# Kernel tuning notes

Hardware: AMD Instinct MI355X
Metric: run time of the kernel (lower is better)

The kernel has to match this reference:

```python
import jax, jax.numpy as jnp
import numpy as np

N_NODES = 100000
N_EDGES = 1600000
IN_DIM = 128
HIDDEN = 128
OUT_DIM = 64


def setup_inputs() -> dict:
    key = jax.random.key(0)
    k_x, k_e, k_w1, k_b1, k_w2, k_b2 = jax.random.split(key, 6)
    x = jax.random.normal(k_x, (N_NODES, IN_DIM), dtype=jnp.float32)
    edge_index = jax.random.randint(k_e, (2, N_EDGES), 0, N_NODES, dtype=jnp.int64)
    # GCNConv weight/bias (glorot-ish scale) and final Linear head
    W1 = jax.random.normal(k_w1, (IN_DIM, HIDDEN), dtype=jnp.float32) / np.sqrt(IN_DIM)
    b1 = jnp.zeros((HIDDEN,), dtype=jnp.float32)
    W2 = jax.random.normal(k_w2, (HIDDEN, OUT_DIM), dtype=jnp.float32) / np.sqrt(HIDDEN)
    b2 = jnp.zeros((OUT_DIM,), dtype=jnp.float32)
    return {"x": x, "W1": W1, "b1": b1, "W2": W2, "b2": b2, "edge_index": edge_index}


def _gcn_conv(x, W, b, src, dst, norm, n_nodes):
    # PyG GCNConv: linear transform, then sym-normalized neighbor aggregation
    h = x @ W                                   # (N, H) dense transform
    msg = h[src] * norm[:, None]                # (E+N, H) gather + scale
    out = jax.ops.segment_sum(msg, dst, num_segments=n_nodes)  # scatter-add
    return out + b


def reference(x, W1, b1, W2, b2, edge_index):
    n = x.shape[0]
    # add self-loops (PyG GCNConv default)
    loop = jnp.arange(n, dtype=edge_index.dtype)
    src = jnp.concatenate([edge_index[0], loop])
    dst = jnp.concatenate([edge_index[1], loop])
    # symmetric normalization D^{-1/2} A D^{-1/2}
    deg = jnp.zeros((n,), dtype=x.dtype).at[dst].add(1.0)
    dinv = jnp.where(deg > 0, jax.lax.rsqrt(jnp.maximum(deg, 1.0)), 0.0)
    norm = dinv[src] * dinv[dst]

    h = _gcn_conv(x, W1, b1, src, dst, norm, n)
    h = jax.nn.relu(h)
    # dropout: identity in eval/inference mode
    return h @ W2 + b2
```

## Files before the change

### kernel.cpp

```cpp
#include <hip/hip_runtime.h>

#define N_NODES 100000
#define N_EDGES 1600000
#define IN_DIM  128
#define HIDDEN  128
#define OUT_DIM 64

#define NB_COARSE ((N_NODES + 255) / 256)
#define EPB 4096
#define NBLK_E ((N_EDGES + EPB - 1) / EPB)
#define GB1 ((N_NODES + 127) / 128)
#define CAP 5120
#define PCAP 6912

typedef __attribute__((ext_vector_type(8))) short bf8_t;
typedef __attribute__((ext_vector_type(4))) float f4_t;

__device__ __forceinline__ ushort f2b(float f) {
    unsigned int u = __float_as_uint(f);
    u += 0x7fffu + ((u >> 16) & 1u);
    return (ushort)(u >> 16);
}
__device__ __forceinline__ float b2f_lo(unsigned int u) { return __uint_as_float(u << 16); }
__device__ __forceinline__ float b2f_hi(unsigned int u) { return __uint_as_float(u & 0xffff0000u); }


__global__ __launch_bounds__(256, 2) void k_fuse1(const int* __restrict__ ei,
                                                  int* __restrict__ cursor,
                                                  unsigned int* __restrict__ part,
                                                  const float* __restrict__ x,
                                                  const float* __restrict__ W1,
                                                  ushort* __restrict__ h) {
    __shared__ __align__(16) ushort smem[2 * 128 * 136];
    int tid = threadIdx.x;

    if (blockIdx.x < NBLK_E) {
        int* lh    = (int*)smem;
        int* lbase = lh + NB_COARSE;
        for (int i = tid; i < NB_COARSE; i += 256) lh[i] = 0;
        __syncthreads();
        int e0 = blockIdx.x * EPB;
        int srcv[EPB / 256], dstv[EPB / 256];
        #pragma unroll
        for (int j = 0; j < EPB / 256; j++) {
            int e = e0 + j * 256 + tid;
            if (e < N_EDGES) {
                srcv[j] = ei[e];
                dstv[j] = ei[N_EDGES + e];
                atomicAdd(&lh[dstv[j] >> 8], 1);
            } else dstv[j] = -1;
        }
        __syncthreads();
        for (int i = tid; i < NB_COARSE; i += 256) {
            int c = lh[i];
            lbase[i] = (c > 0) ? (i * CAP + atomicAdd(&cursor[i], c)) : 0;
            lh[i] = 0;
        }
        __syncthreads();
        #pragma unroll
        for (int j = 0; j < EPB / 256; j++) {
            if (dstv[j] >= 0) {
                int b = dstv[j] >> 8;
                int pos = lbase[b] + atomicAdd(&lh[b], 1);
                part[pos] = ((unsigned int)(dstv[j] & 255) << 24) | (unsigned int)srcv[j];
            }
        }
        return;
    }

    typedef ushort (*tile_t)[136];
    tile_t As = (tile_t)smem;
    tile_t Bs = (tile_t)(smem + 128 * 136);
    int row0 = (blockIdx.x - NBLK_E) * 128;
    const int M = N_NODES;

    #pragma unroll
    for (int i = 0; i < 16; i++) {
        int li = tid + i * 256;
        int r = li >> 5, c4 = li & 31;
        int grow = row0 + r; if (grow > M - 1) grow = M - 1;
        float4 v = *(const float4*)(x + (size_t)grow * 128 + c4 * 4);
        ushort4 o;
        o.x = f2b(v.x); o.y = f2b(v.y); o.z = f2b(v.z); o.w = f2b(v.w);
        *(ushort4*)&As[r][c4 * 4] = o;
    }
    #pragma unroll
    for (int i = 0; i < 16; i++) {
        int li = tid + i * 256;
        int k = li >> 5, n4 = li & 31;
        float4 v = *(const float4*)(W1 + (size_t)k * 128 + n4 * 4);
        Bs[n4 * 4 + 0][k] = f2b(v.x);
        Bs[n4 * 4 + 1][k] = f2b(v.y);
        Bs[n4 * 4 + 2][k] = f2b(v.z);
        Bs[n4 * 4 + 3][k] = f2b(v.w);
    }
    __syncthreads();

    int wave = tid >> 6, lane = tid & 63;
    int lr = lane & 15, lq = lane >> 4;
    int wm0 = (wave & 1) * 64;
    int wn0 = (wave >> 1) * 64;

    f4_t acc[4][4];
    #pragma unroll
    for (int mi = 0; mi < 4; mi++)
        #pragma unroll
        for (int ni = 0; ni < 4; ni++) acc[mi][ni] = (f4_t){0.f, 0.f, 0.f, 0.f};

    #pragma unroll
    for (int kb = 0; kb < 4; kb++) {
        bf8_t af[4], bfr[4];
        #pragma unroll
        for (int mi = 0; mi < 4; mi++)
            af[mi] = *(const bf8_t*)&As[wm0 + mi * 16 + lr][kb * 32 + lq * 8];
        #pragma unroll
        for (int ni = 0; ni < 4; ni++)
            bfr[ni] = *(const bf8_t*)&Bs[wn0 + ni * 16 + lr][kb * 32 + lq * 8];
        #pragma unroll
        for (int mi = 0; mi < 4; mi++)
            #pragma unroll
            for (int ni = 0; ni < 4; ni++)
                acc[mi][ni] = __builtin_amdgcn_mfma_f32_16x16x32_bf16(
                    af[mi], bfr[ni], acc[mi][ni], 0, 0, 0);
    }

    #pragma unroll
    for (int mi = 0; mi < 4; mi++) {
        #pragma unroll
        for (int r = 0; r < 4; r++) {
            int row = row0 + wm0 + mi * 16 + lq * 4 + r;
            if (row < M) {
                #pragma unroll
                for (int ni = 0; ni < 4; ni++)
                    h[(size_t)row * 128 + wn0 + ni * 16 + lr] = f2b(acc[mi][ni][r]);
            }
        }
    }
}


__global__ __launch_bounds__(256) void k_csr(const unsigned int* __restrict__ part,
                                             const int* __restrict__ cursor,
                                             int* __restrict__ offs,
                                             int* __restrict__ pcnt,
                                             float* __restrict__ dinv,
                                             int* __restrict__ ssrc) {
    __shared__ int ldeg[256], lsc[256], lcur[256], sob[256];
    __shared__ unsigned int stage[CAP];
    int t = threadIdx.x;
    int b = blockIdx.x;
    int rbeg = b * CAP;
    int cnt = cursor[b];
    int node0 = b << 8;
    if (b == 0 && t == 0) dinv[N_NODES] = 0.f;
    ldeg[t] = 0;
    __syncthreads();
    for (int i = t; i < cnt; i += 256) {
        unsigned int u = part[rbeg + i];
        stage[i] = u;
        atomicAdd(&ldeg[u >> 24], 1);
    }
    __syncthreads();
    int v = ldeg[t];
    int pv = (v + 7) & ~7;
    lsc[t] = pv;
    __syncthreads();
    for (int off = 1; off < 256; off <<= 1) {
        int add = (t >= off) ? lsc[t - off] : 0;
        __syncthreads();
        lsc[t] += add;
        __syncthreads();
    }
    int ob = b * PCAP + (lsc[t] - pv);
    sob[t] = ob;
    lcur[t] = 0;
    if (node0 + t < N_NODES) {
        offs[node0 + t] = ob;
        pcnt[node0 + t] = pv;
        dinv[node0 + t] = rsqrtf((float)(v + 1));
    }
    __syncthreads();
    for (int i = t; i < cnt; i += 256) {
        unsigned int u = stage[i];
        int d = u >> 24;
        int pos = atomicAdd(&lcur[d], 1);
        ssrc[sob[d] + pos] = (int)(u & 0xFFFFFFu);
    }
    for (int i = v; i < pv; i++) ssrc[ob + i] = N_NODES;
}


__global__ __launch_bounds__(256) void k_agg(const ushort* __restrict__ h,
                                             const int* __restrict__ offs,
                                             const int* __restrict__ pcnt,
                                             const int* __restrict__ ssrc,
                                             const float* __restrict__ dinv,
                                             const float* __restrict__ b1,
                                             ushort* __restrict__ h2) {
    int wave = threadIdx.x >> 6;
    int lane = threadIdx.x & 63;
    int n = blockIdx.x * 4 + wave;
    if (n >= N_NODES) return;

    const unsigned int* hp = (const unsigned int*)h;
    int e0 = offs[n];
    int iters = pcnt[n] >> 3;
    const uint4* ip = (const uint4*)(ssrc + e0);

    float ax0 = 0.f, ay0 = 0.f, ax1 = 0.f, ay1 = 0.f;
    float ax2 = 0.f, ay2 = 0.f, ax3 = 0.f, ay3 = 0.f;
    uint4 i0, i1;
    if (iters > 0) { i0 = ip[0]; i1 = ip[1]; }
    for (int it = 0; it < iters; it++) {
        uint4 nx0 = i0, nx1 = i1;
        if (it + 1 < iters) { nx0 = ip[(it + 1) * 2]; nx1 = ip[(it + 1) * 2 + 1]; }
        float w0 = dinv[i0.x], w1 = dinv[i0.y], w2 = dinv[i0.z], w3 = dinv[i0.w];
        float w4 = dinv[i1.x], w5 = dinv[i1.y], w6 = dinv[i1.z], w7 = dinv[i1.w];
        unsigned int u0 = hp[i0.x * 64 + lane];
        unsigned int u1 = hp[i0.y * 64 + lane];
        unsigned int u2 = hp[i0.z * 64 + lane];
        unsigned int u3 = hp[i0.w * 64 + lane];
        unsigned int u4 = hp[i1.x * 64 + lane];
        unsigned int u5 = hp[i1.y * 64 + lane];
        unsigned int u6 = hp[i1.z * 64 + lane];
        unsigned int u7 = hp[i1.w * 64 + lane];
        ax0 = fmaf(b2f_lo(u0), w0, ax0); ay0 = fmaf(b2f_hi(u0), w0, ay0);
        ax1 = fmaf(b2f_lo(u1), w1, ax1); ay1 = fmaf(b2f_hi(u1), w1, ay1);
        ax2 = fmaf(b2f_lo(u2), w2, ax2); ay2 = fmaf(b2f_hi(u2), w2, ay2);
        ax3 = fmaf(b2f_lo(u3), w3, ax3); ay3 = fmaf(b2f_hi(u3), w3, ay3);
        ax0 = fmaf(b2f_lo(u4), w4, ax0); ay0 = fmaf(b2f_hi(u4), w4, ay0);
        ax1 = fmaf(b2f_lo(u5), w5, ax1); ay1 = fmaf(b2f_hi(u5), w5, ay1);
        ax2 = fmaf(b2f_lo(u6), w6, ax2); ay2 = fmaf(b2f_hi(u6), w6, ay2);
        ax3 = fmaf(b2f_lo(u7), w7, ax3); ay3 = fmaf(b2f_hi(u7), w7, ay3);
        i0 = nx0; i1 = nx1;
    }
    unsigned int us = hp[(size_t)n * 64 + lane];
    float dn = dinv[n];
    float rx = (ax0 + ax1 + ax2 + ax3 + b2f_lo(us) * dn) * dn;
    float ry = (ay0 + ay1 + ay2 + ay3 + b2f_hi(us) * dn) * dn;
    float2 bb = ((const float2*)b1)[lane];
    rx += bb.x; ry += bb.y;
    rx = rx > 0.f ? rx : 0.f;
    ry = ry > 0.f ? ry : 0.f;
    unsigned int o = ((unsigned int)f2b(ry) << 16) | (unsigned int)f2b(rx);
    ((unsigned int*)h2)[(size_t)n * 64 + lane] = o;
}


__global__ __launch_bounds__(256, 2) void k_mfma2(const ushort* __restrict__ A,
                                                  const float* __restrict__ W,
                                                  const float* __restrict__ bias,
                                                  float* __restrict__ C, int M) {
    constexpr int BM = 128, KK = 128, PAD = 8, BN = 64, MF = 2, NF = 4;
    __shared__ ushort As[BM][KK + PAD];
    __shared__ ushort Bs[BN][KK + PAD];

    int tid = threadIdx.x;
    int row0 = blockIdx.x * BM;

    #pragma unroll
    for (int i = 0; i < 8; i++) {
        int li = tid + i * 256;
        int r = li >> 4, c8 = li & 15;
        int grow = row0 + r; if (grow > M - 1) grow = M - 1;
        uint4 v = *(const uint4*)(A + (size_t)grow * KK + c8 * 8);
        *(uint4*)&As[r][c8 * 8] = v;
    }
    #pragma unroll
    for (int i = 0; i < 8; i++) {
        int li = tid + i * 256;
        int k = li >> 4, n4 = li & 15;
        float4 v = *(const float4*)(W + (size_t)k * BN + n4 * 4);
        Bs[n4 * 4 + 0][k] = f2b(v.x);
        Bs[n4 * 4 + 1][k] = f2b(v.y);
        Bs[n4 * 4 + 2][k] = f2b(v.z);
        Bs[n4 * 4 + 3][k] = f2b(v.w);
    }
    __syncthreads();

    int wave = tid >> 6, lane = tid & 63;
    int lr = lane & 15, lq = lane >> 4;
    int wm0 = wave * 32;

    f4_t acc[MF][NF];
    #pragma unroll
    for (int mi = 0; mi < MF; mi++)
        #pragma unroll
        for (int ni = 0; ni < NF; ni++) acc[mi][ni] = (f4_t){0.f, 0.f, 0.f, 0.f};

    #pragma unroll
    for (int kb = 0; kb < 4; kb++) {
        bf8_t af[MF], bfr[NF];
        #pragma unroll
        for (int mi = 0; mi < MF; mi++)
            af[mi] = *(const bf8_t*)&As[wm0 + mi * 16 + lr][kb * 32 + lq * 8];
        #pragma unroll
        for (int ni = 0; ni < NF; ni++)
            bfr[ni] = *(const bf8_t*)&Bs[ni * 16 + lr][kb * 32 + lq * 8];
        #pragma unroll
        for (int mi = 0; mi < MF; mi++)
            #pragma unroll
            for (int ni = 0; ni < NF; ni++)
                acc[mi][ni] = __builtin_amdgcn_mfma_f32_16x16x32_bf16(
                    af[mi], bfr[ni], acc[mi][ni], 0, 0, 0);
    }

    #pragma unroll
    for (int mi = 0; mi < MF; mi++) {
        #pragma unroll
        for (int r = 0; r < 4; r++) {
            int row = row0 + wm0 + mi * 16 + lq * 4 + r;
            if (row < M) {
                #pragma unroll
                for (int ni = 0; ni < NF; ni++) {
                    int col = ni * 16 + lr;
                    C[(size_t)row * BN + col] = acc[mi][ni][r] + bias[col];
                }
            }
        }
    }
}


extern "C" void kernel_launch(void* const* d_in, const int* in_sizes, int n_in,
                              void* d_out, int out_size, void* d_ws, size_t ws_size,
                              hipStream_t stream) {
    const float* x  = (const float*)d_in[0];
    const float* W1 = (const float*)d_in[1];
    const float* b1 = (const float*)d_in[2];
    const float* W2 = (const float*)d_in[3];
    const float* b2 = (const float*)d_in[4];
    const int*   ei = (const int*)d_in[5];
    float* out = (float*)d_out;

    char* w = (char*)d_ws;
    size_t off = 0;
    auto alloc = [&](size_t bytes) -> void* {
        void* p = w + off;
        off += (bytes + 255) & ~(size_t)255;
        return p;
    };
    ushort* h      = (ushort*)alloc((size_t)(N_NODES + 1) * HIDDEN * 2);
    ushort* h2     = (ushort*)alloc((size_t)N_NODES * HIDDEN * 2);
    float* dinv    = (float*)alloc((size_t)(N_NODES + 1) * 4);
    int*   offs    = (int*)alloc((size_t)N_NODES * 4);
    int*   pcnt    = (int*)alloc((size_t)N_NODES * 4);
    int*   ssrc    = (int*)alloc((size_t)NB_COARSE * PCAP * 4);
    unsigned int* part = (unsigned int*)alloc((size_t)NB_COARSE * CAP * 4);
    int*   cursor  = (int*)alloc((size_t)NB_COARSE * 4);

    hipMemsetAsync(cursor, 0, (size_t)NB_COARSE * 4, stream);
    k_fuse1<<<NBLK_E + GB1, 256, 0, stream>>>(ei, cursor, part, x, W1, h);
    k_csr<<<NB_COARSE, 256, 0, stream>>>(part, cursor, offs, pcnt, dinv, ssrc);
    k_agg<<<(N_NODES + 3) / 4, 256, 0, stream>>>(h, offs, pcnt, ssrc, dinv, b1, h2);
    k_mfma2<<<GB1, 256, 0, stream>>>(h2, W2, b2, out, N_NODES);
}
```

Before: 225.9 us.

## Fuse neighbor aggregation with output linear layer via per-block MFMA

Merges the aggregation kernel and the final GEMM into one kernel. Each block aggregates 16 nodes (4 per wave), writes the ReLU'd bf16 rows to shared memory, then runs a 16x64 MFMA against W2, which every block loads and converts. This removes the h2 intermediate round trip through global memory (about 25 MB written and read) and one kernel launch. In exchange, every block redoes the W2 load and bf16 conversion, each wave handles four nodes in sequence, and the grid relies on N_NODES being divisible by 16.

```diff
diff --git a/kernel.cpp b/kernel.cpp
--- a/kernel.cpp
+++ b/kernel.cpp
@@ -190,134 +190,95 @@
 }
 
 
-__global__ __launch_bounds__(256) void k_agg(const ushort* __restrict__ h,
-                                             const int* __restrict__ offs,
-                                             const int* __restrict__ pcnt,
-                                             const int* __restrict__ ssrc,
-                                             const float* __restrict__ dinv,
-                                             const float* __restrict__ b1,
-                                             ushort* __restrict__ h2) {
-    int wave = threadIdx.x >> 6;
-    int lane = threadIdx.x & 63;
-    int n = blockIdx.x * 4 + wave;
-    if (n >= N_NODES) return;
-
-    const unsigned int* hp = (const unsigned int*)h;
-    int e0 = offs[n];
-    int iters = pcnt[n] >> 3;
-    const uint4* ip = (const uint4*)(ssrc + e0);
-
-    float ax0 = 0.f, ay0 = 0.f, ax1 = 0.f, ay1 = 0.f;
-    float ax2 = 0.f, ay2 = 0.f, ax3 = 0.f, ay3 = 0.f;
-    uint4 i0, i1;
-    if (iters > 0) { i0 = ip[0]; i1 = ip[1]; }
-    for (int it = 0; it < iters; it++) {
-        uint4 nx0 = i0, nx1 = i1;
-        if (it + 1 < iters) { nx0 = ip[(it + 1) * 2]; nx1 = ip[(it + 1) * 2 + 1]; }
-        float w0 = dinv[i0.x], w1 = dinv[i0.y], w2 = dinv[i0.z], w3 = dinv[i0.w];
-        float w4 = dinv[i1.x], w5 = dinv[i1.y], w6 = dinv[i1.z], w7 = dinv[i1.w];
-        unsigned int u0 = hp[i0.x * 64 + lane];
-        unsigned int u1 = hp[i0.y * 64 + lane];
-        unsigned int u2 = hp[i0.z * 64 + lane];
-        unsigned int u3 = hp[i0.w * 64 + lane];
-        unsigned int u4 = hp[i1.x * 64 + lane];
-        unsigned int u5 = hp[i1.y * 64 + lane];
-        unsigned int u6 = hp[i1.z * 64 + lane];
-        unsigned int u7 = hp[i1.w * 64 + lane];
-        ax0 = fmaf(b2f_lo(u0), w0, ax0); ay0 = fmaf(b2f_hi(u0), w0, ay0);
-        ax1 = fmaf(b2f_lo(u1), w1, ax1); ay1 = fmaf(b2f_hi(u1), w1, ay1);
-        ax2 = fmaf(b2f_lo(u2), w2, ax2); ay2 = fmaf(b2f_hi(u2), w2, ay2);
-        ax3 = fmaf(b2f_lo(u3), w3, ax3); ay3 = fmaf(b2f_hi(u3), w3, ay3);
-        ax0 = fmaf(b2f_lo(u4), w4, ax0); ay0 = fmaf(b2f_hi(u4), w4, ay0);
-        ax1 = fmaf(b2f_lo(u5), w5, ax1); ay1 = fmaf(b2f_hi(u5), w5, ay1);
-        ax2 = fmaf(b2f_lo(u6), w6, ax2); ay2 = fmaf(b2f_hi(u6), w6, ay2);
-        ax3 = fmaf(b2f_lo(u7), w7, ax3); ay3 = fmaf(b2f_hi(u7), w7, ay3);
-        i0 = nx0; i1 = nx1;
-    }
-    unsigned int us = hp[(size_t)n * 64 + lane];
-    float dn = dinv[n];
-    float rx = (ax0 + ax1 + ax2 + ax3 + b2f_lo(us) * dn) * dn;
-    float ry = (ay0 + ay1 + ay2 + ay3 + b2f_hi(us) * dn) * dn;
-    float2 bb = ((const float2*)b1)[lane];
-    rx += bb.x; ry += bb.y;
-    rx = rx > 0.f ? rx : 0.f;
-    ry = ry > 0.f ? ry : 0.f;
-    unsigned int o = ((unsigned int)f2b(ry) << 16) | (unsigned int)f2b(rx);
-    ((unsigned int*)h2)[(size_t)n * 64 + lane] = o;
-}
-
-
-__global__ __launch_bounds__(256, 2) void k_mfma2(const ushort* __restrict__ A,
-                                                  const float* __restrict__ W,
-                                                  const float* __restrict__ bias,
-                                                  float* __restrict__ C, int M) {
-    constexpr int BM = 128, KK = 128, PAD = 8, BN = 64, MF = 2, NF = 4;
-    __shared__ ushort As[BM][KK + PAD];
-    __shared__ ushort Bs[BN][KK + PAD];
-
+__global__ __launch_bounds__(256, 6) void k_agg2(const ushort* __restrict__ h,
+                                                 const int* __restrict__ offs,
+                                                 const int* __restrict__ pcnt,
+                                                 const int* __restrict__ ssrc,
+                                                 const float* __restrict__ dinv,
+                                                 const float* __restrict__ b1,
+                                                 const float* __restrict__ W2,
+                                                 const float* __restrict__ b2,
+                                                 float* __restrict__ out) {
+    __shared__ ushort As[16][136];
+    __shared__ ushort Bs[64][136];
     int tid = threadIdx.x;
-    int row0 = blockIdx.x * BM;
-
-    #pragma unroll
-    for (int i = 0; i < 8; i++) {
-        int li = tid + i * 256;
-        int r = li >> 4, c8 = li & 15;
-        int grow = row0 + r; if (grow > M - 1) grow = M - 1;
-        uint4 v = *(const uint4*)(A + (size_t)grow * KK + c8 * 8);
-        *(uint4*)&As[r][c8 * 8] = v;
-    }
+    int wave = tid >> 6, lane = tid & 63;
+    int base = blockIdx.x * 16;
+
     #pragma unroll
     for (int i = 0; i < 8; i++) {
         int li = tid + i * 256;
         int k = li >> 4, n4 = li & 15;
-        float4 v = *(const float4*)(W + (size_t)k * BN + n4 * 4);
+        float4 v = *(const float4*)(W2 + (size_t)k * 64 + n4 * 4);
         Bs[n4 * 4 + 0][k] = f2b(v.x);
         Bs[n4 * 4 + 1][k] = f2b(v.y);
         Bs[n4 * 4 + 2][k] = f2b(v.z);
         Bs[n4 * 4 + 3][k] = f2b(v.w);
     }
-    __syncthreads();
-
-    int wave = tid >> 6, lane = tid & 63;
+
+    const unsigned int* hp = (const unsigned int*)h;
+    float2 bb = ((const float2*)b1)[lane];
+
+    #pragma unroll 1
+    for (int j = 0; j < 4; j++) {
+        int r = wave * 4 + j;
+        int n = base + r;
+        int e0 = offs[n];
+        int iters = pcnt[n] >> 3;
+        const uint4* ip = (const uint4*)(ssrc + e0);
+
+        float ax0 = 0.f, ay0 = 0.f, ax1 = 0.f, ay1 = 0.f;
+        float ax2 = 0.f, ay2 = 0.f, ax3 = 0.f, ay3 = 0.f;
+        uint4 i0, i1;
+        if (iters > 0) { i0 = ip[0]; i1 = ip[1]; }
+        for (int it = 0; it < iters; it++) {
+            uint4 nx0 = i0, nx1 = i1;
+            if (it + 1 < iters) { nx0 = ip[(it + 1) * 2]; nx1 = ip[(it + 1) * 2 + 1]; }
+            float w0 = dinv[i0.x], w1 = dinv[i0.y], w2 = dinv[i0.z], w3 = dinv[i0.w];
+            float w4 = dinv[i1.x], w5 = dinv[i1.y], w6 = dinv[i1.z], w7 = dinv[i1.w];
+            unsigned int u0 = hp[i0.x * 64 + lane];
+            unsigned int u1 = hp[i0.y * 64 + lane];
+            unsigned int u2 = hp[i0.z * 64 + lane];
+            unsigned int u3 = hp[i0.w * 64 + lane];
+            unsigned int u4 = hp[i1.x * 64 + lane];
+            unsigned int u5 = hp[i1.y * 64 + lane];
+            unsigned int u6 = hp[i1.z * 64 + lane];
+            unsigned int u7 = hp[i1.w * 64 + lane];
+            ax0 = fmaf(b2f_lo(u0), w0, ax0); ay0 = fmaf(b2f_hi(u0), w0, ay0);
+            ax1 = fmaf(b2f_lo(u1), w1, ax1); ay1 = fmaf(b2f_hi(u1), w1, ay1);
+            ax2 = fmaf(b2f_lo(u2), w2, ax2); ay2 = fmaf(b2f_hi(u2), w2, ay2);
+            ax3 = fmaf(b2f_lo(u3), w3, ax3); ay3 = fmaf(b2f_hi(u3), w3, ay3);
+            ax0 = fmaf(b2f_lo(u4), w4, ax0); ay0 = fmaf(b2f_hi(u4), w4, ay0);
+            ax1 = fmaf(b2f_lo(u5), w5, ax1); ay1 = fmaf(b2f_hi(u5), w5, ay1);
+            ax2 = fmaf(b2f_lo(u6), w6, ax2); ay2 = fmaf(b2f_hi(u6), w6, ay2);
+            ax3 = fmaf(b2f_lo(u7), w7, ax3); ay3 = fmaf(b2f_hi(u7), w7, ay3);
+            i0 = nx0; i1 = nx1;
+        }
+        unsigned int us = hp[(size_t)n * 64 + lane];
+        float dn = dinv[n];
+        float rx = (ax0 + ax1 + ax2 + ax3 + b2f_lo(us) * dn) * dn + bb.x;
+        float ry = (ay0 + ay1 + ay2 + ay3 + b2f_hi(us) * dn) * dn + bb.y;
+        rx = rx > 0.f ? rx : 0.f;
+        ry = ry > 0.f ? ry : 0.f;
+        *(unsigned int*)&As[r][lane * 2] =
+            ((unsigned int)f2b(ry) << 16) | (unsigned int)f2b(rx);
+    }
+    __syncthreads();
+
     int lr = lane & 15, lq = lane >> 4;
-    int wm0 = wave * 32;
-
-    f4_t acc[MF][NF];
-    #pragma unroll
-    for (int mi = 0; mi < MF; mi++)
-        #pragma unroll
-        for (int ni = 0; ni < NF; ni++) acc[mi][ni] = (f4_t){0.f, 0.f, 0.f, 0.f};
-
+    f4_t acc = (f4_t){0.f, 0.f, 0.f, 0.f};
     #pragma unroll
     for (int kb = 0; kb < 4; kb++) {
-        bf8_t af[MF], bfr[NF];
-        #pragma unroll
-        for (int mi = 0; mi < MF; mi++)
-            af[mi] = *(const bf8_t*)&As[wm0 + mi * 16 + lr][kb * 32 + lq * 8];
-        #pragma unroll
-        for (int ni = 0; ni < NF; ni++)
-            bfr[ni] = *(const bf8_t*)&Bs[ni * 16 + lr][kb * 32 + lq * 8];
-        #pragma unroll
-        for (int mi = 0; mi < MF; mi++)
-            #pragma unroll
-            for (int ni = 0; ni < NF; ni++)
-                acc[mi][ni] = __builtin_amdgcn_mfma_f32_16x16x32_bf16(
-                    af[mi], bfr[ni], acc[mi][ni], 0, 0, 0);
-    }
-
-    #pragma unroll
-    for (int mi = 0; mi < MF; mi++) {
-        #pragma unroll
-        for (int r = 0; r < 4; r++) {
-            int row = row0 + wm0 + mi * 16 + lq * 4 + r;
-            if (row < M) {
-                #pragma unroll
-                for (int ni = 0; ni < NF; ni++) {
-                    int col = ni * 16 + lr;
-                    C[(size_t)row * BN + col] = acc[mi][ni][r] + bias[col];
-                }
-            }
-        }
+        bf8_t af = *(const bf8_t*)&As[lr][kb * 32 + lq * 8];
+        bf8_t bf = *(const bf8_t*)&Bs[wave * 16 + lr][kb * 32 + lq * 8];
+        acc = __builtin_amdgcn_mfma_f32_16x16x32_bf16(af, bf, acc, 0, 0, 0);
+    }
+    int col = wave * 16 + lr;
+    float bv = b2[col];
+    #pragma unroll
+    for (int r = 0; r < 4; r++) {
+        int node = base + lq * 4 + r;
+        out[(size_t)node * 64 + col] = acc[r] + bv;
     }
 }
 
@@ -341,7 +302,6 @@
         return p;
     };
     ushort* h      = (ushort*)alloc((size_t)(N_NODES + 1) * HIDDEN * 2);
-    ushort* h2     = (ushort*)alloc((size_t)N_NODES * HIDDEN * 2);
     float* dinv    = (float*)alloc((size_t)(N_NODES + 1) * 4);
     int*   offs    = (int*)alloc((size_t)N_NODES * 4);
     int*   pcnt    = (int*)alloc((size_t)N_NODES * 4);
@@ -352,6 +312,5 @@
     hipMemsetAsync(cursor, 0, (size_t)NB_COARSE * 4, stream);
     k_fuse1<<<NBLK_E + GB1, 256, 0, stream>>>(ei, cursor, part, x, W1, h);
     k_csr<<<NB_COARSE, 256, 0, stream>>>(part, cursor, offs, pcnt, dinv, ssrc);
-    k_agg<<<(N_NODES + 3) / 4, 256, 0, stream>>>(h, offs, pcnt, ssrc, dinv, b1, h2);
-    k_mfma2<<<GB1, 256, 0, stream>>>(h2, W2, b2, out, N_NODES);
-}
+    k_agg2<<<N_NODES / 16, 256, 0, stream>>>(h, offs, pcnt, ssrc, dinv, b1, W2, b2, out);
+}
```

Result: faster. 219.9 us (-2.6%).
